# Kernel tuning notes

Hardware: AMD Instinct MI355X
Metric: run time of the kernel (lower is better)

The kernel has to match this reference:

```python
import jax, jax.numpy as jnp
import numpy as np

LEAKY_SLOPE = 0.01  # torch nn.LeakyReLU default


def leaky_relu(x):
    return jnp.where(x >= 0, x, LEAKY_SLOPE * x)


def rgcn_conv(x, edge_index, edge_type, w_rel, w_root, b_conv):
    # PyG RGCNConv: out = x @ W_root + b + sum_r mean_{edges of rel r into i}(x_src @ W_r)
    n = x.shape[0]
    src, dst = edge_index[0], edge_index[1]
    out = x @ w_root + b_conv
    num_rel = w_rel.shape[0]
    for r in range(num_rel):  # small fixed relation count
        mask = (edge_type == r)
        msg = x[src] @ w_rel[r]                      # [E, H]
        msg = jnp.where(mask[:, None], msg, 0.0)
        agg = jax.ops.segment_sum(msg, dst, num_segments=n)          # [N, H]
        cnt = jax.ops.segment_sum(mask.astype(x.dtype), dst, num_segments=n)
        out = out + agg / jnp.maximum(cnt, 1.0)[:, None]             # mean aggr
    return out


def setup_inputs() -> dict:
    key = jax.random.key(0)
    ks = jax.random.split(key, 10)
    N, E, D_IN, H, OUT, R = 50000, 600000, 768, 128, 3, 2
    s_in = 1.0 / np.sqrt(D_IN)
    s_h = 1.0 / np.sqrt(H)
    return {
        "feature": jax.random.normal(ks[0], (N, D_IN), dtype=jnp.float32),
        "edge_index": jax.random.randint(ks[1], (2, E), 0, N, dtype=jnp.int64),
        "edge_type": jax.random.randint(ks[2], (E,), 0, R, dtype=jnp.int64),
        "w_in": jax.random.uniform(ks[3], (D_IN, H), jnp.float32, -s_in, s_in),
        "b_in": jax.random.uniform(ks[4], (H,), jnp.float32, -s_in, s_in),
        "w_rel": jax.random.uniform(ks[5], (R, H, H), jnp.float32, -s_h, s_h),
        "w_root": jax.random.uniform(ks[6], (H, H), jnp.float32, -s_h, s_h),
        "b_conv": jnp.zeros((H,), jnp.float32),
        "w_out": jax.random.uniform(ks[7], (H, OUT), jnp.float32, -s_h, s_h),
        "b_out": jax.random.uniform(ks[8], (OUT,), jnp.float32, -s_h, s_h),
    }


def reference(feature, edge_index, edge_type, w_in, b_in, w_rel, w_root, b_conv, w_out, b_out):
    x = leaky_relu(feature @ w_in + b_in)
    # NOTE: original forward applies rgcn1 twice (shared weights); dropout is
    # identity at inference; rgcn2/linear_relu_output1 are unused.
    x = rgcn_conv(x, edge_index, edge_type, w_rel, w_root, b_conv)
    x = rgcn_conv(x, edge_index, edge_type, w_rel, w_root, b_conv)
    return x @ w_out + b_out
```

## Files before the change

kernel.cpp:

```cpp
#include <hip/hip_runtime.h>

#define H 128
#define CAP 64

typedef _Float16 f16x8 __attribute__((ext_vector_type(8)));
typedef _Float16 f16x4 __attribute__((ext_vector_type(4)));
typedef float    f32x4 __attribute__((ext_vector_type(4)));

__global__ __launch_bounds__(256) void hist_fill(const int* __restrict__ src,
    const int* __restrict__ dst, const int* __restrict__ et,
    int* __restrict__ cnt, int* __restrict__ elist, int E, int N)
{
    int e = blockIdx.x * 256 + threadIdx.x;
    if (e >= E) return;
    int s = src[e], d = dst[e], t = et[e];
    int b = t * N + d;
    int pos = atomicAdd(&cnt[b], 1);
    if (pos < CAP) elist[(size_t)b * CAP + pos] = s;
}

__global__ __launch_bounds__(256) void cvt_feat(const float* __restrict__ A,
    _Float16* __restrict__ A16, long long total8)
{
    long long i = (long long)blockIdx.x * 256 + threadIdx.x;
    long long stride = (long long)gridDim.x * 256;
    for (; i < total8; i += stride) {
        float4 v0 = *(const float4*)(A + i * 8);
        float4 v1 = *(const float4*)(A + i * 8 + 4);
        f16x8 o;
        o[0] = (_Float16)v0.x; o[1] = (_Float16)v0.y;
        o[2] = (_Float16)v0.z; o[3] = (_Float16)v0.w;
        o[4] = (_Float16)v1.x; o[5] = (_Float16)v1.y;
        o[6] = (_Float16)v1.z; o[7] = (_Float16)v1.w;
        *(f16x8*)(A16 + i * 8) = o;
    }
}

__global__ __launch_bounds__(256) void prep_w(const float* __restrict__ w_in,
    const float* __restrict__ w_root, const float* __restrict__ w_rel,
    _Float16* __restrict__ wInT, _Float16* __restrict__ wcatT, int K)
{
    int idx = blockIdx.x * 256 + threadIdx.x;
    int tot1 = K * H;
    if (idx < tot1) {
        int k = idx >> 7, c = idx & 127;
        int o = ((k >> 3) << 10) + (c << 3) + (k & 7);
        wInT[o] = (_Float16)w_in[idx];
    } else {
        int i2 = idx - tot1;
        if (i2 < H * 384) {
            int c = i2 / 384, k = i2 - c * 384;
            float v;
            if (k < 128)      v = w_root[(size_t)k * H + c];
            else if (k < 256) v = w_rel[(size_t)(k - 128) * H + c];
            else              v = w_rel[(size_t)H * H + (size_t)(k - 256) * H + c];
            wcatT[i2] = (_Float16)v;
        }
    }
}

__global__ __launch_bounds__(256) void prep_fin(const float* __restrict__ w_root,
    const float* __restrict__ w_rel, const float* __restrict__ b_conv,
    const float* __restrict__ w_out, const float* __restrict__ b_out,
    float* __restrict__ wfin, float* __restrict__ bfin, int OUT)
{
    int idx = blockIdx.x * 256 + threadIdx.x;
    int nw = 3 * H * OUT;
    if (idx < nw) {
        int mk = idx / OUT, c = idx - mk * OUT;
        int m = mk >> 7, k = mk & 127;
        const float* W = (m == 0) ? w_root : (w_rel + (size_t)(m - 1) * H * H);
        float s = 0.f;
        for (int j = 0; j < H; j++)
            s += W[(size_t)k * H + j] * w_out[(size_t)j * OUT + c];
        wfin[(size_t)mk * OUT + c] = s;
    } else if (idx < nw + OUT) {
        int c = idx - nw;
        float s = b_out[c];
        for (int j = 0; j < H; j++) s += b_conv[j] * w_out[(size_t)j * OUT + c];
        bfin[c] = s;
    }
}

__global__ __launch_bounds__(256, 3) void gemm_big(const _Float16* __restrict__ A16,
    const _Float16* __restrict__ WP, const float* __restrict__ bias,
    _Float16* __restrict__ C16, int M, int K, int ldc)
{
    __shared__ _Float16 As[2][8192];

    const int tid = threadIdx.x;
    const int w   = tid >> 6;
    const int l   = tid & 63;
    const int l15 = l & 15;
    const int q   = l >> 4;
    const int brow = blockIdx.x * 64;
    const int wr   = w * 16;

    const int r4  = l >> 4;
    const int c16 = l & 15;

    const _Float16* bp = WP + ((size_t)q * H + l15) * 8;

    float bj[8];
#pragma unroll
    for (int j = 0; j < 8; j++) bj[j] = bias[j * 16 + l15];

    f32x4 acc[8];
    const f32x4 z4 = {0.f, 0.f, 0.f, 0.f};
#pragma unroll
    for (int j = 0; j < 8; j++) acc[j] = z4;

    const int chunks = K / 128;
    f16x8 st[4];

    {
        const _Float16* apc = A16 + c16 * 8;
#pragma unroll
        for (int i = 0; i < 4; i++) {
            int gr = brow + wr + r4 + i * 4; if (gr >= M) gr = M - 1;
            st[i] = *(const f16x8*)(apc + (size_t)gr * K);
        }
#pragma unroll
        for (int i = 0; i < 4; i++) {
            int row = wr + r4 + i * 4;
            *(f16x8*)&As[0][c16 * 512 + ((row ^ (c16 & 7)) << 3)] = st[i];
        }
    }
    __syncthreads();

    for (int c = 0; c < chunks; c++) {
        const bool more = (c + 1) < chunks;
        if (more) {
            const _Float16* apc = A16 + (c + 1) * 128 + c16 * 8;
#pragma unroll
            for (int i = 0; i < 4; i++) {
                int gr = brow + wr + r4 + i * 4; if (gr >= M) gr = M - 1;
                st[i] = *(const f16x8*)(apc + (size_t)gr * K);
            }
        }
        {
            const _Float16* __restrict__ buf = As[c & 1];
#pragma unroll
            for (int ks = 0; ks < 4; ks++) {
                const int sl = ks * 4 + q;
                f16x8 af = *(const f16x8*)&buf[sl * 512 + (((wr + l15) ^ (sl & 7)) << 3)];
                const _Float16* bks = bp + (size_t)(c * 4 + ks) * 4096;
                f16x8 bf[8];
#pragma unroll
                for (int j = 0; j < 8; j++) bf[j] = *(const f16x8*)(bks + j * 128);
#pragma unroll
                for (int j = 0; j < 8; j++)
                    acc[j] = __builtin_amdgcn_mfma_f32_16x16x32_f16(af, bf[j], acc[j], 0, 0, 0);
            }
        }
        if (more) {
            _Float16* __restrict__ buf = As[(c + 1) & 1];
#pragma unroll
            for (int i = 0; i < 4; i++) {
                int row = wr + r4 + i * 4;
                *(f16x8*)&buf[c16 * 512 + ((row ^ (c16 & 7)) << 3)] = st[i];
            }
        }
        __syncthreads();
    }

#pragma unroll
    for (int rg = 0; rg < 4; rg++) {
        int row = brow + wr + q * 4 + rg;
        if (row < M) {
#pragma unroll
            for (int j = 0; j < 8; j++) {
                float v = acc[j][rg] + bj[j];
                v = (v >= 0.f) ? v : 0.01f * v;
                C16[(size_t)row * ldc + j * 16 + l15] = (_Float16)v;
            }
        }
    }
}

template<int MODE>
__global__ __launch_bounds__(256) void gather_k(const _Float16* __restrict__ X,
    int ldx, _Float16* __restrict__ Mout, const int* __restrict__ elist,
    const int* __restrict__ cnt, int N,
    const float* __restrict__ wfin, const float* __restrict__ bfin,
    float* __restrict__ out)
{
    int wv = blockIdx.x * 4 + (threadIdx.x >> 6);
    int l  = threadIdx.x & 63;
    if (wv >= N) return;

    const int eo   = l >> 4;
    const int e2   = eo & 1;
    const int half = l >> 5;
    const int c8   = (l & 15) * 8;

    int dr = cnt[(size_t)half * N + wv];
    int d  = dr < CAP ? dr : CAP;
    float inv = dr > 0 ? 1.f / (float)dr : 0.f;
    const int* lst = elist + ((size_t)half * N + wv) * CAP;

    float acc[8];
#pragma unroll
    for (int j = 0; j < 8; j++) acc[j] = 0.f;

    const f16x8 zv = {};
    for (int p = e2; p < d; p += 8) {
        int p1 = p + 2, p2 = p + 4, p3 = p + 6;
        int s0 = lst[p];
        f16x8 v0 = *(const f16x8*)&X[(size_t)s0 * ldx + c8];
        f16x8 v1 = zv, v2 = zv, v3 = zv;
        if (p1 < d) { int s = lst[p1]; v1 = *(const f16x8*)&X[(size_t)s * ldx + c8]; }
        if (p2 < d) { int s = lst[p2]; v2 = *(const f16x8*)&X[(size_t)s * ldx + c8]; }
        if (p3 < d) { int s = lst[p3]; v3 = *(const f16x8*)&X[(size_t)s * ldx + c8]; }
#pragma unroll
        for (int j = 0; j < 8; j++)
            acc[j] += (float)v0[j] + (float)v1[j] + (float)v2[j] + (float)v3[j];
    }

#pragma unroll
    for (int j = 0; j < 8; j++) {
        acc[j] += __shfl_xor(acc[j], 16);
        acc[j] *= inv;
    }

    if (MODE == 0) {
        if (eo == 0 || eo == 2) {
            f16x8 o;
#pragma unroll
            for (int j = 0; j < 8; j++) o[j] = (_Float16)acc[j];
            *(f16x8*)&Mout[(size_t)wv * 256 + half * 128 + c8] = o;
        }
    } else {
        float p0 = 0.f, p1 = 0.f, p2 = 0.f;
        if (eo == 1) {
            f16x8 xv = *(const f16x8*)&X[(size_t)wv * ldx + c8];
#pragma unroll
            for (int j = 0; j < 8; j++) {
                float xf = (float)xv[j];
                const float* wr = wfin + (size_t)(c8 + j) * 3;
                p0 += xf * wr[0]; p1 += xf * wr[1]; p2 += xf * wr[2];
            }
        } else if (eo == 0 || eo == 2) {
            const float* wb = wfin + (size_t)(eo == 0 ? 1 : 2) * H * 3;
#pragma unroll
            for (int j = 0; j < 8; j++) {
                const float* wr = wb + (size_t)(c8 + j) * 3;
                p0 += acc[j] * wr[0]; p1 += acc[j] * wr[1]; p2 += acc[j] * wr[2];
            }
        }
#pragma unroll
        for (int off = 1; off <= 32; off <<= 1) {
            p0 += __shfl_xor(p0, off);
            p1 += __shfl_xor(p1, off);
            p2 += __shfl_xor(p2, off);
        }
        if (l == 0) {
            out[(size_t)wv * 3 + 0] = p0 + bfin[0];
            out[(size_t)wv * 3 + 1] = p1 + bfin[1];
            out[(size_t)wv * 3 + 2] = p2 + bfin[2];
        }
    }
}

__global__ __launch_bounds__(512) void gemm_cat(const _Float16* __restrict__ X1,
    const _Float16* __restrict__ Mt, const _Float16* __restrict__ WT,
    const float* __restrict__ bias, _Float16* __restrict__ X2, int M, int mtiles)
{
    const int w   = threadIdx.x >> 6;
    const int l   = threadIdx.x & 63;
    const int l15 = l & 15;
    const int q   = l >> 4;
    const int col = w * 16 + l15;

    f16x8 bf[12];
    {
        const _Float16* wpp = WT + (size_t)col * 384 + q * 8;
#pragma unroll
        for (int c = 0; c < 12; c++) bf[c] = *(const f16x8*)(wpp + c * 32);
    }
    const float bj = bias[col];

    int t = blockIdx.x;
    if (t >= mtiles) return;
    f16x8 xf[12];
    {
        const _Float16* xp = X1 + ((size_t)t * 16 + l15) * 128 + q * 8;
        const _Float16* mp = Mt + ((size_t)t * 16 + l15) * 256 + q * 8;
#pragma unroll
        for (int c = 0; c < 4; c++) xf[c] = *(const f16x8*)(xp + c * 32);
#pragma unroll
        for (int c = 4; c < 12; c++) xf[c] = *(const f16x8*)(mp + (c - 4) * 32);
    }

    const f32x4 z4 = {0.f, 0.f, 0.f, 0.f};
    while (true) {
        int tn = t + gridDim.x;
        bool more = tn < mtiles;
        f16x8 xnf[12];
        if (more) {
            const _Float16* xp = X1 + ((size_t)tn * 16 + l15) * 128 + q * 8;
            const _Float16* mp = Mt + ((size_t)tn * 16 + l15) * 256 + q * 8;
#pragma unroll
            for (int c = 0; c < 4; c++) xnf[c] = *(const f16x8*)(xp + c * 32);
#pragma unroll
            for (int c = 4; c < 12; c++) xnf[c] = *(const f16x8*)(mp + (c - 4) * 32);
        }

        f32x4 a0 = z4;
#pragma unroll
        for (int c = 0; c < 12; c++)
            a0 = __builtin_amdgcn_mfma_f32_16x16x32_f16(xf[c], bf[c], a0, 0, 0, 0);

#pragma unroll
        for (int rg = 0; rg < 4; rg++) {
            int row = t * 16 + q * 4 + rg;
            if (row < M) X2[(size_t)row * 128 + col] = (_Float16)(a0[rg] + bj);
        }
        if (!more) break;
        t = tn;
#pragma unroll
        for (int c = 0; c < 12; c++) xf[c] = xnf[c];
    }
}

__global__ __launch_bounds__(256) void proj_generic(const _Float16* __restrict__ X2,
    const _Float16* __restrict__ Mt, const float* __restrict__ wfin,
    const float* __restrict__ bfin, float* __restrict__ out, int N, int OUT)
{
    int row = blockIdx.x * 4 + (threadIdx.x >> 6);
    int l = threadIdx.x & 63;
    if (row >= N) return;
    float xv[6];
#pragma unroll
    for (int i = 0; i < 6; i++) {
        int k = l * 6 + i;
        xv[i] = (k < 128) ? (float)X2[(size_t)row * 128 + k]
                          : (float)Mt[(size_t)row * 256 + (k - 128)];
    }
    for (int c = 0; c < OUT; c++) {
        float p = 0.f;
#pragma unroll
        for (int i = 0; i < 6; i++) p += xv[i] * wfin[(size_t)(l * 6 + i) * OUT + c];
        for (int off = 32; off > 0; off >>= 1) p += __shfl_down(p, off);
        if (l == 0) out[(size_t)row * OUT + c] = p + bfin[c];
    }
}

extern "C" void kernel_launch(void* const* d_in, const int* in_sizes, int n_in,
                              void* d_out, int out_size, void* d_ws, size_t ws_size,
                              hipStream_t stream) {
    const float* feature = (const float*)d_in[0];
    const int*   ei      = (const int*)d_in[1];
    const int*   et      = (const int*)d_in[2];
    const float* w_in    = (const float*)d_in[3];
    const float* b_in    = (const float*)d_in[4];
    const float* w_rel   = (const float*)d_in[5];
    const float* w_root  = (const float*)d_in[6];
    const float* b_conv  = (const float*)d_in[7];
    const float* w_out   = (const float*)d_in[8];
    const float* b_out   = (const float*)d_in[9];

    const int HH   = in_sizes[4];
    const int D_IN = in_sizes[3] / HH;
    const int N    = in_sizes[0] / D_IN;
    const int E    = in_sizes[1] / 2;
    const int OUT  = in_sizes[9];

    char* base = (char*)d_ws;
    _Float16* A16   = (_Float16*)base;
    _Float16* wInT  = A16 + (size_t)N * D_IN;
    _Float16* wcatT = wInT + (size_t)D_IN * HH;
    _Float16* X1    = wcatT + (size_t)HH * 384;
    _Float16* X2    = X1 + (size_t)N * HH;
    _Float16* Mt    = X2 + (size_t)N * HH;
    float* wfin     = (float*)(Mt + (size_t)N * 256);
    float* bfin     = wfin + (size_t)3 * HH * (OUT > 0 ? OUT : 1);
    int* cnt        = (int*)(bfin + ((OUT + 3) & ~3));
    int* elist      = cnt + (size_t)2 * N;

    hipMemsetAsync(cnt, 0, sizeof(int) * (size_t)2 * N, stream);
    prep_w<<<(D_IN * HH + HH * 384 + 255) / 256, 256, 0, stream>>>(
        w_in, w_root, w_rel, wInT, wcatT, D_IN);
    prep_fin<<<(3 * HH * OUT + OUT + 255) / 256, 256, 0, stream>>>(
        w_root, w_rel, b_conv, w_out, b_out, wfin, bfin, OUT);
    hist_fill<<<(E + 255) / 256, 256, 0, stream>>>(ei, ei + E, et, cnt, elist, E, N);

    long long total8 = (long long)N * D_IN / 8;
    cvt_feat<<<2048, 256, 0, stream>>>(feature, A16, total8);
    gemm_big<<<(N + 63) / 64, 256, 0, stream>>>(A16, wInT, b_in, X1, N, D_IN, HH);

    const int mtiles  = (N + 15) / 16;
    const int gblocks = (N + 3) / 4;

    gather_k<0><<<gblocks, 256, 0, stream>>>(X1, 128, Mt, elist, cnt, N,
                                             nullptr, nullptr, nullptr);
    gemm_cat<<<1024, 512, 0, stream>>>(X1, Mt, wcatT, b_conv, X2, N, mtiles);
    if (OUT == 3) {
        gather_k<1><<<gblocks, 256, 0, stream>>>(X2, 128, nullptr, elist, cnt, N,
                                                 wfin, bfin, (float*)d_out);
    } else {
        gather_k<0><<<gblocks, 256, 0, stream>>>(X2, 128, Mt, elist, cnt, N,
                                                 nullptr, nullptr, nullptr);
        proj_generic<<<gblocks, 256, 0, stream>>>(X2, Mt, wfin, bfin,
                                                  (float*)d_out, N, OUT);
    }
}
```

Baseline: 462.1 us.

## Fuse fp32-to-fp16 feature conversion into input GEMM using direct global-to-LDS loads

Removes the separate cvt_feat pass that converted the 50000x768 fp32 features to fp16, and has gemm_big read fp32 directly via global_load_lds into a swizzled fp32 LDS buffer, converting to fp16 when forming MFMA operands. This saves one full write and re-read of the fp16 copy of the feature matrix. In exchange the LDS footprint doubles (64KB), so launch bounds drop to 2 blocks per CU, and the conversion moves into the inner loop.

```diff
diff --git a/kernel.cpp b/kernel.cpp
--- a/kernel.cpp
+++ b/kernel.cpp
@@ -4,7 +4,6 @@
 #define CAP 64
 
 typedef _Float16 f16x8 __attribute__((ext_vector_type(8)));
-typedef _Float16 f16x4 __attribute__((ext_vector_type(4)));
 typedef float    f32x4 __attribute__((ext_vector_type(4)));
 
 __global__ __launch_bounds__(256) void hist_fill(const int* __restrict__ src,
@@ -17,23 +16,6 @@
     int b = t * N + d;
     int pos = atomicAdd(&cnt[b], 1);
     if (pos < CAP) elist[(size_t)b * CAP + pos] = s;
-}
-
-__global__ __launch_bounds__(256) void cvt_feat(const float* __restrict__ A,
-    _Float16* __restrict__ A16, long long total8)
-{
-    long long i = (long long)blockIdx.x * 256 + threadIdx.x;
-    long long stride = (long long)gridDim.x * 256;
-    for (; i < total8; i += stride) {
-        float4 v0 = *(const float4*)(A + i * 8);
-        float4 v1 = *(const float4*)(A + i * 8 + 4);
-        f16x8 o;
-        o[0] = (_Float16)v0.x; o[1] = (_Float16)v0.y;
-        o[2] = (_Float16)v0.z; o[3] = (_Float16)v0.w;
-        o[4] = (_Float16)v1.x; o[5] = (_Float16)v1.y;
-        o[6] = (_Float16)v1.z; o[7] = (_Float16)v1.w;
-        *(f16x8*)(A16 + i * 8) = o;
-    }
 }
 
 __global__ __launch_bounds__(256) void prep_w(const float* __restrict__ w_in,
@@ -82,11 +64,18 @@
     }
 }
 
-__global__ __launch_bounds__(256, 3) void gemm_big(const _Float16* __restrict__ A16,
+__device__ __forceinline__ f16x8 cvt8(float4 v0, float4 v1) {
+    f16x8 t;
+    t[0] = (_Float16)v0.x; t[1] = (_Float16)v0.y; t[2] = (_Float16)v0.z; t[3] = (_Float16)v0.w;
+    t[4] = (_Float16)v1.x; t[5] = (_Float16)v1.y; t[6] = (_Float16)v1.z; t[7] = (_Float16)v1.w;
+    return t;
+}
+
+__global__ __launch_bounds__(256, 2) void gemm_big(const float* __restrict__ A,
     const _Float16* __restrict__ WP, const float* __restrict__ bias,
     _Float16* __restrict__ C16, int M, int K, int ldc)
 {
-    __shared__ _Float16 As[2][8192];
+    __shared__ float As[2][4][2048];
 
     const int tid = threadIdx.x;
     const int w   = tid >> 6;
@@ -96,8 +85,8 @@
     const int brow = blockIdx.x * 64;
     const int wr   = w * 16;
 
-    const int r4  = l >> 4;
-    const int c16 = l & 15;
+    const int lh  = l >> 5;
+    const int l31 = l & 31;
 
     const _Float16* bp = WP + ((size_t)q * H + l15) * 8;
 
@@ -111,58 +100,49 @@
     for (int j = 0; j < 8; j++) acc[j] = z4;
 
     const int chunks = K / 128;
-    f16x8 st[4];
-
-    {
-        const _Float16* apc = A16 + c16 * 8;
-#pragma unroll
-        for (int i = 0; i < 4; i++) {
-            int gr = brow + wr + r4 + i * 4; if (gr >= M) gr = M - 1;
-            st[i] = *(const f16x8*)(apc + (size_t)gr * K);
-        }
-#pragma unroll
-        for (int i = 0; i < 4; i++) {
-            int row = wr + r4 + i * 4;
-            *(f16x8*)&As[0][c16 * 512 + ((row ^ (c16 & 7)) << 3)] = st[i];
-        }
-    }
+
+#define STAGE(c, nbuf)                                                          \
+    {                                                                           \
+        _Pragma("unroll")                                                       \
+        for (int i = 0; i < 8; i++) {                                           \
+            int r  = 2 * i + lh;                                                \
+            int gr = brow + wr + r; if (gr >= M) gr = M - 1;                    \
+            int cg = l31 ^ (r & 7);                                             \
+            const float* ga = A + (size_t)gr * K + (c) * 128 + cg * 4;          \
+            __builtin_amdgcn_global_load_lds(                                   \
+                (const __attribute__((address_space(1))) void*)ga,              \
+                (__attribute__((address_space(3))) void*)&As[nbuf][w][i * 256], \
+                16, 0, 0);                                                      \
+        }                                                                       \
+    }
+
+    STAGE(0, 0);
     __syncthreads();
 
     for (int c = 0; c < chunks; c++) {
-        const bool more = (c + 1) < chunks;
-        if (more) {
-            const _Float16* apc = A16 + (c + 1) * 128 + c16 * 8;
-#pragma unroll
-            for (int i = 0; i < 4; i++) {
-                int gr = brow + wr + r4 + i * 4; if (gr >= M) gr = M - 1;
-                st[i] = *(const f16x8*)(apc + (size_t)gr * K);
-            }
-        }
-        {
-            const _Float16* __restrict__ buf = As[c & 1];
-#pragma unroll
-            for (int ks = 0; ks < 4; ks++) {
-                const int sl = ks * 4 + q;
-                f16x8 af = *(const f16x8*)&buf[sl * 512 + (((wr + l15) ^ (sl & 7)) << 3)];
-                const _Float16* bks = bp + (size_t)(c * 4 + ks) * 4096;
-                f16x8 bf[8];
-#pragma unroll
-                for (int j = 0; j < 8; j++) bf[j] = *(const f16x8*)(bks + j * 128);
-#pragma unroll
-                for (int j = 0; j < 8; j++)
-                    acc[j] = __builtin_amdgcn_mfma_f32_16x16x32_f16(af, bf[j], acc[j], 0, 0, 0);
-            }
-        }
-        if (more) {
-            _Float16* __restrict__ buf = As[(c + 1) & 1];
-#pragma unroll
-            for (int i = 0; i < 4; i++) {
-                int row = wr + r4 + i * 4;
-                *(f16x8*)&buf[c16 * 512 + ((row ^ (c16 & 7)) << 3)] = st[i];
-            }
+        if (c + 1 < chunks) STAGE(c + 1, (c + 1) & 1);
+
+        const float* wbuf = As[c & 1][w];
+#pragma unroll
+        for (int ks = 0; ks < 4; ks++) {
+            const int sl = ks * 4 + q;
+            const int xr = l15 & 7;
+            const int p0 = (2 * sl) ^ xr;
+            const int p1 = (2 * sl + 1) ^ xr;
+            float4 lo = *(const float4*)&wbuf[l15 * 128 + p0 * 4];
+            float4 hi = *(const float4*)&wbuf[l15 * 128 + p1 * 4];
+            f16x8 af = cvt8(lo, hi);
+            const _Float16* bks = bp + (size_t)(c * 4 + ks) * 4096;
+            f16x8 bf[8];
+#pragma unroll
+            for (int j = 0; j < 8; j++) bf[j] = *(const f16x8*)(bks + j * 128);
+#pragma unroll
+            for (int j = 0; j < 8; j++)
+                acc[j] = __builtin_amdgcn_mfma_f32_16x16x32_f16(af, bf[j], acc[j], 0, 0, 0);
         }
         __syncthreads();
     }
+#undef STAGE
 
 #pragma unroll
     for (int rg = 0; rg < 4; rg++) {
@@ -367,8 +347,7 @@
     const int OUT  = in_sizes[9];
 
     char* base = (char*)d_ws;
-    _Float16* A16   = (_Float16*)base;
-    _Float16* wInT  = A16 + (size_t)N * D_IN;
+    _Float16* wInT  = (_Float16*)base;
     _Float16* wcatT = wInT + (size_t)D_IN * HH;
     _Float16* X1    = wcatT + (size_t)HH * 384;
     _Float16* X2    = X1 + (size_t)N * HH;
@@ -385,9 +364,7 @@
         w_root, w_rel, b_conv, w_out, b_out, wfin, bfin, OUT);
     hist_fill<<<(E + 255) / 256, 256, 0, stream>>>(ei, ei + E, et, cnt, elist, E, N);
 
-    long long total8 = (long long)N * D_IN / 8;
-    cvt_feat<<<2048, 256, 0, stream>>>(feature, A16, total8);
-    gemm_big<<<(N + 63) / 64, 256, 0, stream>>>(A16, wInT, b_in, X1, N, D_IN, HH);
+    gemm_big<<<(N + 63) / 64, 256, 0, stream>>>(feature, wInT, b_in, X1, N, D_IN, HH);
 
     const int mtiles  = (N + 15) / 16;
     const int gblocks = (N + 3) / 4;
```

New measurement: 440.1 us. 1.05x faster.
